# Optimization experiments

Hardware: AMD Instinct MI355X
Metric: run time of the kernel (lower is better)

Reference implementation:

```python
import jax, jax.numpy as jnp
import numpy as np

B, N, C_IN, C_Z, H = 1, 2048, 128, 16, 4
C = C_IN // H  # 32 per-head dim
QB, WL, WR = 32, 48, 80  # AF3 local atom attention: 32-query blocks, 128-key window


def _ln(x, eps=1e-5):
    m = jnp.mean(x, axis=-1, keepdims=True)
    v = jnp.mean((x - m) ** 2, axis=-1, keepdims=True)
    return (x - m) * jax.lax.rsqrt(v + eps)


def setup_inputs() -> dict:
    key = jax.random.key(0)
    ks = iter(jax.random.split(key, 32))
    def rn(shape, scale=0.02):
        return jax.random.normal(next(ks), shape, jnp.float32) * scale
    d = {}
    d['single_act'] = jax.random.normal(next(ks), (B, N, C_IN), jnp.float32)
    d['pair_act'] = jax.random.normal(next(ks), (B, N, N, C_Z), jnp.float32)
    d['single_cond'] = jax.random.normal(next(ks), (B, N, C_IN), jnp.float32)
    qi = jnp.arange(N)[:, None]
    kj = jnp.arange(N)[None, :]
    blk = (qi // QB) * QB
    d['block_mask'] = (kj >= blk - WL) & (kj < blk + WR)
    # AdaptiveLayerNorm params for q and k branches
    for p in ('q', 'k'):
        d[f'lns_{p}'] = jnp.ones((C_IN,), jnp.float32)       # LN(cond) scale (no bias)
        d[f'Wgate_{p}'] = rn((C_IN, C_IN))
        d[f'bgate_{p}'] = jnp.zeros((C_IN,), jnp.float32)
        d[f'Wskip_{p}'] = rn((C_IN, C_IN))
    d['lnz_w'] = jnp.ones((C_Z,), jnp.float32)               # layer_norm_z weight (bias=False)
    d['Wq'] = rn((C_IN, C_IN)); d['bq'] = jnp.zeros((C_IN,), jnp.float32)
    d['Wk'] = rn((C_IN, C_IN))
    d['Wv'] = rn((C_IN, C_IN))
    d['Wg'] = rn((C_IN, C_IN))
    d['Wb'] = rn((C_Z, H))
    # AdaptiveZeroInit: gated output projection, gate bias init -2
    d['Wo'] = rn((C_IN, C_IN))
    d['Wgs'] = rn((C_IN, C_IN))
    d['bgs'] = jnp.full((C_IN,), -2.0, jnp.float32)
    return d


def reference(single_act, pair_act, single_cond, block_mask,
              lns_q, Wgate_q, bgate_q, Wskip_q,
              lns_k, Wgate_k, bgate_k, Wskip_k,
              lnz_w, Wq, bq, Wk, Wv, Wg, Wb, Wo, Wgs, bgs):
    def adaln(x, s, lnsw, Wgt, bgt, Wsk):
        xn = _ln(x)                 # LN without affine
        sn = _ln(s) * lnsw          # LN with scale, no bias
        return jax.nn.sigmoid(sn @ Wgt + bgt) * xn + sn @ Wsk

    a_q = adaln(single_act, single_cond, lns_q, Wgate_q, bgate_q, Wskip_q)
    a_k = adaln(single_act, single_cond, lns_k, Wgate_k, bgate_k, Wskip_k)
    z = _ln(pair_act) * lnz_w                     # [B,N,N,Cz]

    q = (a_q @ Wq + bq).reshape(B, N, H, C)
    k = (a_k @ Wk).reshape(B, N, H, C)
    v = (a_k @ Wv).reshape(B, N, H, C)
    g = (a_q @ Wg).reshape(B, N, H, C)
    bias = z @ Wb                                 # [B,N,N,H]

    scores = jnp.einsum('bihc,bjhc->bhij', q, k) * (1.0 / np.sqrt(C).astype(np.float32))
    scores = scores + jnp.transpose(bias, (0, 3, 1, 2))
    scores = jnp.where(block_mask[None, None], scores, jnp.float32(-1e9))
    attn = jax.nn.softmax(scores, axis=-1)
    o = jnp.einsum('bhij,bjhc->bihc', attn, v)    # [B,N,H,C]
    o = (jax.nn.sigmoid(g) * o).reshape(B, N, C_IN)
    # AdaptiveZeroInit: sigmoid(Linear(cond)) * LinearNoBias(o)
    return jax.nn.sigmoid(single_cond @ Wgs + bgs) * (o @ Wo)
```

## Files before the change

### kernel.cpp

```cpp
#include <hip/hip_runtime.h>
#include <hip/hip_bf16.h>

#define NTOK 2048

typedef __attribute__((ext_vector_type(8))) short short8_t;
typedef __attribute__((ext_vector_type(4))) float f32x4;

__device__ __forceinline__ float bu2f(unsigned short u) {
  unsigned int x = ((unsigned int)u) << 16; float f; __builtin_memcpy(&f, &x, 4); return f;
}
__device__ __forceinline__ unsigned short f2bu(float f) {
  __hip_bfloat16 h = __float2bfloat16(f);
  unsigned short u; __builtin_memcpy(&u, &h, 2); return u;
}
__device__ __forceinline__ float sigm(float x) { return 1.0f / (1.0f + __expf(-x)); }
__device__ __forceinline__ uint4 pack8(const float* v) {
  unsigned short u[8];
#pragma unroll
  for (int i = 0; i < 8; ++i) u[i] = f2bu(v[i]);
  uint4 r; __builtin_memcpy(&r, u, 16); return r;
}
__device__ __forceinline__ short8_t pk8s(const float* v) {
  unsigned short u[8];
#pragma unroll
  for (int i = 0; i < 8; ++i) u[i] = f2bu(v[i]);
  short8_t r; __builtin_memcpy(&r, u, 16); return r;
}

__device__ __forceinline__ short8_t wfrag(const float* __restrict__ W,
                                          const float* __restrict__ lns,
                                          int ko, int n) {
  float v[8];
#pragma unroll
  for (int i = 0; i < 8; ++i) v[i] = W[(size_t)(ko + i) * 128 + n];
  if (lns) {
    float4 l0 = *(const float4*)(lns + ko);
    float4 l1 = *(const float4*)(lns + ko + 4);
    v[0] *= l0.x; v[1] *= l0.y; v[2] *= l0.z; v[3] *= l0.w;
    v[4] *= l1.x; v[5] *= l1.y; v[6] *= l1.z; v[7] *= l1.w;
  }
  return pk8s(v);
}

__device__ __forceinline__ void gemm_dw(const unsigned short* a_lds,
                                        const float* __restrict__ W,
                                        const float* __restrict__ lns,
                                        int lm, int kg, int wv, f32x4 acc[2][2]) {
  const int xa = (lm & 7) << 3;
#pragma unroll
  for (int ks = 0; ks < 4; ++ks) {
    const int ko = ks * 32 + kg * 8;
    short8_t av[2], bv[2];
#pragma unroll
    for (int mi = 0; mi < 2; ++mi)
      av[mi] = *(const short8_t*)&a_lds[(mi * 16 + lm) * 128 + (ko ^ xa)];
#pragma unroll
    for (int ni = 0; ni < 2; ++ni)
      bv[ni] = wfrag(W, lns, ko, (wv * 2 + ni) * 16 + lm);
#pragma unroll
    for (int mi = 0; mi < 2; ++mi)
#pragma unroll
      for (int ni = 0; ni < 2; ++ni)
        acc[mi][ni] = __builtin_amdgcn_mfma_f32_16x16x32_bf16(av[mi], bv[ni], acc[mi][ni], 0, 0, 0);
  }
}

__global__ __launch_bounds__(256) void bias_proj_kernel(
    const float* __restrict__ act, const float* __restrict__ cond,
    const float* __restrict__ lns_q, const float* __restrict__ lns_k,
    const float* __restrict__ WgQ, const float* __restrict__ WsQ,
    const float* __restrict__ WgK, const float* __restrict__ WsK,
    const float* __restrict__ Wq, const float* __restrict__ Wk,
    const float* __restrict__ Wv, const float* __restrict__ Wg,
    const float* __restrict__ Wgs,
    const float* __restrict__ bgate_q, const float* __restrict__ bgate_k,
    const float* __restrict__ bq, const float* __restrict__ bgs,
    const float* __restrict__ pair, const float* __restrict__ lnz_w,
    const float* __restrict__ Wb,
    unsigned short* __restrict__ q_b, unsigned short* __restrict__ k_b,
    unsigned short* __restrict__ vt_b, unsigned short* __restrict__ gsig_b,
    unsigned short* __restrict__ gs_b, unsigned short* __restrict__ bias_h)
{
  __shared__ unsigned short a_lds[32 * 128];
  __shared__ unsigned short xn_lds[32 * 136];
  __shared__ unsigned short a2_lds[32 * 128];
  __shared__ float lw[16];
  __shared__ float wbz[16][4];
  const int tid = threadIdx.x;
  const int bid = blockIdx.x;

  if (bid < 1024) {
    if (tid < 16) lw[tid] = lnz_w[tid];
    if (tid < 64) wbz[tid >> 2][tid & 3] = Wb[tid];
    __syncthreads();
    const int idx = bid * 256 + tid;
    const int i = idx >> 7, jw = idx & 127;
    const int j = ((i >> 5) << 5) - 48 + jw;
    float bo[4] = {-1e9f, -1e9f, -1e9f, -1e9f};
    if (j >= 0 && j < NTOK) {
      const float4* p = (const float4*)(pair + ((size_t)i * NTOK + j) * 16);
      float4 z0 = p[0], z1 = p[1], z2 = p[2], z3 = p[3];
      float z[16] = {z0.x, z0.y, z0.z, z0.w, z1.x, z1.y, z1.z, z1.w,
                     z2.x, z2.y, z2.z, z2.w, z3.x, z3.y, z3.z, z3.w};
      float s = 0.f, ss = 0.f;
#pragma unroll
      for (int c = 0; c < 16; ++c) { s += z[c]; ss += z[c]*z[c]; }
      const float m = s * (1.f/16.f), v = ss * (1.f/16.f) - m*m;
      const float r = rsqrtf(v + 1e-5f);
      bo[0] = bo[1] = bo[2] = bo[3] = 0.f;
#pragma unroll
      for (int c = 0; c < 16; ++c) {
        const float zn = (z[c] - m) * r * lw[c];
        bo[0] += zn * wbz[c][0]; bo[1] += zn * wbz[c][1];
        bo[2] += zn * wbz[c][2]; bo[3] += zn * wbz[c][3];
      }
    }
#pragma unroll
    for (int h = 0; h < 4; ++h)
      bias_h[(size_t)h * (NTOK * 128) + idx] = f2bu(bo[h]);
    return;
  }

  const int bb = bid - 1024;
  const int br = bb / 64;
  const int rt = bb % 64;
  const int row0 = rt * 32;
  const int l = tid & 63, wv = tid >> 6;
  const int lm = l & 15, kg = l >> 4;

  {
    const int r = tid >> 3;
    const int c0 = (tid & 7) << 4;
    float xv[16], cv[16];
    const float4* ap = (const float4*)(act + (size_t)(row0 + r) * 128 + c0);
    const float4* cp = (const float4*)(cond + (size_t)(row0 + r) * 128 + c0);
#pragma unroll
    for (int i = 0; i < 4; ++i) {
      float4 a4 = ap[i], b4 = cp[i];
      xv[4*i+0]=a4.x; xv[4*i+1]=a4.y; xv[4*i+2]=a4.z; xv[4*i+3]=a4.w;
      cv[4*i+0]=b4.x; cv[4*i+1]=b4.y; cv[4*i+2]=b4.z; cv[4*i+3]=b4.w;
    }
    float sx=0.f, sxx=0.f, sc=0.f, scc=0.f;
#pragma unroll
    for (int i = 0; i < 16; ++i) { sx+=xv[i]; sxx+=xv[i]*xv[i]; sc+=cv[i]; scc+=cv[i]*cv[i]; }
#pragma unroll
    for (int m = 1; m < 8; m <<= 1) {
      sx += __shfl_xor(sx, m); sxx += __shfl_xor(sxx, m);
      sc += __shfl_xor(sc, m); scc += __shfl_xor(scc, m);
    }
    const float mx = sx * (1.f/128.f), vx = sxx*(1.f/128.f) - mx*mx;
    const float mc = sc * (1.f/128.f), vc = scc*(1.f/128.f) - mc*mc;
    const float rx = rsqrtf(vx + 1e-5f), rc = rsqrtf(vc + 1e-5f);
    float xo[16], so[16];
#pragma unroll
    for (int i = 0; i < 16; ++i) { xo[i] = (xv[i]-mx)*rx; so[i] = (cv[i]-mc)*rc; }
    const int x = (r & 7) << 3;
    if (br == 4) {
      *(uint4*)&a_lds[r * 128 + (c0 ^ x)] = pack8(cv);
      *(uint4*)&a_lds[r * 128 + ((c0 + 8) ^ x)] = pack8(cv + 8);
    } else {
      *(uint4*)&a_lds[r * 128 + (c0 ^ x)] = pack8(so);
      *(uint4*)&a_lds[r * 128 + ((c0 + 8) ^ x)] = pack8(so + 8);
      *(uint4*)&xn_lds[r * 136 + c0] = pack8(xo);
      *(uint4*)&xn_lds[r * 136 + c0 + 8] = pack8(xo + 8);
    }
  }
  __syncthreads();

  if (br == 4) {
    f32x4 acc[2][2] = {};
    gemm_dw(a_lds, Wgs, nullptr, lm, kg, wv, acc);
    float bgv[2];
#pragma unroll
    for (int ni = 0; ni < 2; ++ni) bgv[ni] = bgs[(wv * 2 + ni) * 16 + lm];
#pragma unroll
    for (int mi = 0; mi < 2; ++mi)
#pragma unroll
      for (int ni = 0; ni < 2; ++ni)
#pragma unroll
        for (int r = 0; r < 4; ++r) {
          const int rl = mi * 16 + kg * 4 + r;
          const int n = (wv * 2 + ni) * 16 + lm;
          gs_b[(size_t)(row0 + rl) * 128 + n] = f2bu(sigm(acc[mi][ni][r] + bgv[ni]));
        }
    return;
  }

  const bool useq = (br < 2);
  const float* Wgt = useq ? WgQ : WgK;
  const float* Wsk = useq ? WsQ : WsK;
  const float* lns = useq ? lns_q : lns_k;
  const float* bg  = useq ? bgate_q : bgate_k;

  f32x4 ag[2][2] = {}, as2[2][2] = {};
  gemm_dw(a_lds, Wgt, lns, lm, kg, wv, ag);
  gemm_dw(a_lds, Wsk, lns, lm, kg, wv, as2);
  {
    float bgv[2];
#pragma unroll
    for (int ni = 0; ni < 2; ++ni) bgv[ni] = bg[(wv * 2 + ni) * 16 + lm];
#pragma unroll
    for (int mi = 0; mi < 2; ++mi)
#pragma unroll
      for (int ni = 0; ni < 2; ++ni)
#pragma unroll
        for (int r = 0; r < 4; ++r) {
          const int rl = mi * 16 + kg * 4 + r;
          const int n = (wv * 2 + ni) * 16 + lm;
          const float gate = sigm(ag[mi][ni][r] + bgv[ni]);
          const float a = gate * bu2f(xn_lds[rl * 136 + n]) + as2[mi][ni][r];
          a2_lds[rl * 128 + (n ^ ((rl & 7) << 3))] = f2bu(a);
        }
  }
  __syncthreads();

  const float* Wout = (br == 0) ? Wq : (br == 1) ? Wg : (br == 2) ? Wk : Wv;
  f32x4 ao[2][2] = {};
  gemm_dw(a2_lds, Wout, nullptr, lm, kg, wv, ao);

  if (br == 3) {
#pragma unroll
    for (int mi = 0; mi < 2; ++mi)
#pragma unroll
      for (int ni = 0; ni < 2; ++ni) {
        const int n = (wv * 2 + ni) * 16 + lm;
        const int tok0 = row0 + mi * 16 + kg * 4;
        ushort4 o;
        o.x = f2bu(ao[mi][ni][0]); o.y = f2bu(ao[mi][ni][1]);
        o.z = f2bu(ao[mi][ni][2]); o.w = f2bu(ao[mi][ni][3]);
        *(ushort4*)(vt_b + (size_t)n * NTOK + tok0) = o;
      }
    return;
  }
  const float scale = 0.17677669529663687f;
  float bqv[2] = {0.f, 0.f};
  if (br == 0) {
#pragma unroll
    for (int ni = 0; ni < 2; ++ni) bqv[ni] = bq[(wv * 2 + ni) * 16 + lm];
  }
  unsigned short* dst = (br == 0) ? q_b : (br == 1) ? gsig_b : k_b;
#pragma unroll
  for (int mi = 0; mi < 2; ++mi)
#pragma unroll
    for (int ni = 0; ni < 2; ++ni)
#pragma unroll
      for (int r = 0; r < 4; ++r) {
        const int rl = mi * 16 + kg * 4 + r;
        const int n = (wv * 2 + ni) * 16 + lm;
        float v = ao[mi][ni][r];
        if (br == 0) v = (v + bqv[ni]) * scale;
        else if (br == 1) v = sigm(v);
        dst[(size_t)(row0 + rl) * 128 + n] = f2bu(v);
      }
}

__global__ __launch_bounds__(256) void attn_kernel(
    const unsigned short* __restrict__ q_b, const unsigned short* __restrict__ k_b,
    const unsigned short* __restrict__ vt_b, const unsigned short* __restrict__ gsig_b,
    const unsigned short* __restrict__ bias_h, unsigned short* __restrict__ o_b)
{
  __shared__ unsigned short k_lds[128 * 64];
  __shared__ unsigned short vt[32 * 128];
  __shared__ unsigned short p_lds[32 * 128];
  __shared__ unsigned short q_lds[32 * 64];
  __shared__ unsigned short bias_lds[32 * 136];
  __shared__ float mxlds[4][32];
  __shared__ float smlds[4][32];
  __shared__ f32x4 op[16][64];
  const int tid = threadIdx.x;
  const int h = blockIdx.x & 3, b = blockIdx.x >> 2;
  const int j0 = b * 32 - 48;
  const int l = tid & 63, wv = tid >> 6;
  const int lm = l & 15, kg = l >> 4;

  {
    const int r = tid >> 3, c0 = (tid & 7) << 2;
    ushort4 v = *(const ushort4*)(q_b + (size_t)(b * 32 + r) * 128 + h * 32 + c0);
    *(ushort4*)&q_lds[r * 64 + (c0 ^ ((r & 7) << 3))] = v;
  }
  {
    const int r = tid >> 3, c0 = (tid & 7) << 4;
    const uint4* g = (const uint4*)(bias_h + (size_t)h * (NTOK * 128) + (size_t)(b * 32 + r) * 128 + c0);
    uint4 v0 = g[0], v1 = g[1];
    *(uint4*)&bias_lds[r * 136 + c0] = v0;
    *(uint4*)&bias_lds[r * 136 + c0 + 8] = v1;
  }
  {
    const int jw = tid >> 1, cb = (tid & 1) << 4;
    const int j = j0 + jw;
    uint4 kv0 = {0,0,0,0}, kv1 = {0,0,0,0};
    if (j >= 0 && j < NTOK) {
      const uint4* gk = (const uint4*)(k_b + (size_t)j * 128 + h * 32 + cb);
      kv0 = gk[0]; kv1 = gk[1];
    }
    const int xk = (jw & 7) << 3;
    *(uint4*)&k_lds[jw * 64 + (cb ^ xk)] = kv0;
    *(uint4*)&k_lds[jw * 64 + ((cb + 8) ^ xk)] = kv1;
  }
  {
    const int c = tid >> 3, koff = (tid & 7) << 4;
    const int j = j0 + koff;
    uint4 v0 = {0,0,0,0}, v1 = {0,0,0,0};
    if (j >= 0 && j + 15 < NTOK) {
      const uint4* gv = (const uint4*)(vt_b + (size_t)(h * 32 + c) * NTOK + j);
      v0 = gv[0]; v1 = gv[1];
    }
    const int xc = (c & 7) << 3;
    *(uint4*)&vt[c * 128 + (koff ^ xc)] = v0;
    *(uint4*)&vt[c * 128 + ((koff + 8) ^ xc)] = v1;
  }
  __syncthreads();

  f32x4 sc[2][2] = {};
  {
    const int xa = (lm & 7) << 3;
    short8_t aq[2], bk[2];
#pragma unroll
    for (int mi = 0; mi < 2; ++mi)
      aq[mi] = *(const short8_t*)&q_lds[(mi * 16 + lm) * 64 + ((kg * 8) ^ xa)];
#pragma unroll
    for (int ni = 0; ni < 2; ++ni) {
      const int key = (wv * 2 + ni) * 16 + lm;
      bk[ni] = *(const short8_t*)&k_lds[key * 64 + ((kg * 8) ^ ((key & 7) << 3))];
    }
#pragma unroll
    for (int mi = 0; mi < 2; ++mi)
#pragma unroll
      for (int ni = 0; ni < 2; ++ni)
        sc[mi][ni] = __builtin_amdgcn_mfma_f32_16x16x32_bf16(aq[mi], bk[ni], sc[mi][ni], 0, 0, 0);
  }
  float sv[2][2][4];
#pragma unroll
  for (int mi = 0; mi < 2; ++mi)
#pragma unroll
    for (int ni = 0; ni < 2; ++ni)
#pragma unroll
      for (int r = 0; r < 4; ++r) {
        const int q = mi * 16 + kg * 4 + r;
        const int key = (wv * 2 + ni) * 16 + lm;
        sv[mi][ni][r] = sc[mi][ni][r] + bu2f(bias_lds[q * 136 + key]);
      }
#pragma unroll
  for (int mi = 0; mi < 2; ++mi)
#pragma unroll
    for (int r = 0; r < 4; ++r) {
      float m0 = fmaxf(sv[mi][0][r], sv[mi][1][r]);
#pragma unroll
      for (int msk = 1; msk < 16; msk <<= 1) m0 = fmaxf(m0, __shfl_xor(m0, msk));
      if (lm == 0) mxlds[wv][mi * 16 + kg * 4 + r] = m0;
    }
  __syncthreads();
#pragma unroll
  for (int mi = 0; mi < 2; ++mi)
#pragma unroll
    for (int r = 0; r < 4; ++r) {
      const int q = mi * 16 + kg * 4 + r;
      const float m = fmaxf(fmaxf(mxlds[0][q], mxlds[1][q]), fmaxf(mxlds[2][q], mxlds[3][q]));
      float s = 0.f;
#pragma unroll
      for (int ni = 0; ni < 2; ++ni) {
        const float e = __expf(sv[mi][ni][r] - m);
        const int key = (wv * 2 + ni) * 16 + lm;
        p_lds[q * 128 + ((key & 7) | ((key & 120) ^ ((q & 7) << 3)))] = f2bu(e);
        s += e;
      }
#pragma unroll
      for (int msk = 1; msk < 16; msk <<= 1) s += __shfl_xor(s, msk);
      if (lm == 0) smlds[wv][q] = s;
    }
  f32x4 oacc[2][2] = {};
  {
    const int key0 = wv * 32 + kg * 8;
    short8_t pa[2], vbf[2];
#pragma unroll
    for (int mi = 0; mi < 2; ++mi) {
      const int q = mi * 16 + lm;
      pa[mi] = *(const short8_t*)&p_lds[q * 128 + (key0 ^ ((q & 7) << 3))];
    }
#pragma unroll
    for (int ct = 0; ct < 2; ++ct) {
      const int c = ct * 16 + lm;
      vbf[ct] = *(const short8_t*)&vt[c * 128 + (key0 ^ ((c & 7) << 3))];
    }
#pragma unroll
    for (int mi = 0; mi < 2; ++mi)
#pragma unroll
      for (int ct = 0; ct < 2; ++ct)
        oacc[mi][ct] = __builtin_amdgcn_mfma_f32_16x16x32_bf16(pa[mi], vbf[ct], oacc[mi][ct], 0, 0, 0);
  }
#pragma unroll
  for (int mi = 0; mi < 2; ++mi)
#pragma unroll
    for (int ct = 0; ct < 2; ++ct)
      op[wv * 4 + mi * 2 + ct][l] = oacc[mi][ct];
  __syncthreads();
  {
    const int q = tid >> 3, c0 = (tid & 7) << 2;
    const int mt = q >> 4, g = (q >> 2) & 3, r = q & 3;
    const float tot = smlds[0][q] + smlds[1][q] + smlds[2][q] + smlds[3][q];
    const float inv = 1.f / tot;
    ushort4 gg = *(const ushort4*)(gsig_b + (size_t)(b * 32 + q) * 128 + h * 32 + c0);
    unsigned short gga[4] = {gg.x, gg.y, gg.z, gg.w};
    unsigned short outa[4];
#pragma unroll
    for (int i2 = 0; i2 < 4; ++i2) {
      const int c = c0 + i2;
      const int ct = c >> 4, lane = g * 16 + (c & 15);
      float s = 0.f;
#pragma unroll
      for (int w2 = 0; w2 < 4; ++w2)
        s += ((const float*)&op[w2 * 4 + mt * 2 + ct][lane])[r];
      outa[i2] = f2bu(s * inv * bu2f(gga[i2]));
    }
    ushort4 ov; ov.x = outa[0]; ov.y = outa[1]; ov.z = outa[2]; ov.w = outa[3];
    *(ushort4*)(o_b + (size_t)(b * 32 + q) * 128 + h * 32 + c0) = ov;
  }
}

__global__ __launch_bounds__(256) void out_kernel(
    const float* __restrict__ Wo, const unsigned short* __restrict__ o_b,
    const unsigned short* __restrict__ gs_b, float* __restrict__ out)
{
  __shared__ unsigned short a_lds[16 * 128];
  const int tid = threadIdx.x;
  const int row0 = blockIdx.x * 16;
  const int l = tid & 63, wv = tid >> 6;
  const int lm = l & 15, kg = l >> 4;
  {
    const int r = tid >> 4, c0 = (tid & 15) << 3;
    uint4 v = *(const uint4*)(o_b + (size_t)(row0 + r) * 128 + c0);
    *(uint4*)&a_lds[r * 128 + (c0 ^ ((r & 7) << 3))] = v;
  }
  __syncthreads();
  f32x4 acc[2] = {};
  const int xa = (lm & 7) << 3;
#pragma unroll
  for (int ks = 0; ks < 4; ++ks) {
    const int ko = ks * 32 + kg * 8;
    short8_t av = *(const short8_t*)&a_lds[lm * 128 + (ko ^ xa)];
#pragma unroll
    for (int ni = 0; ni < 2; ++ni) {
      short8_t bv = wfrag(Wo, nullptr, ko, (wv * 2 + ni) * 16 + lm);
      acc[ni] = __builtin_amdgcn_mfma_f32_16x16x32_bf16(av, bv, acc[ni], 0, 0, 0);
    }
  }
#pragma unroll
  for (int ni = 0; ni < 2; ++ni)
#pragma unroll
    for (int r = 0; r < 4; ++r) {
      const int rl = kg * 4 + r;
      const int n = (wv * 2 + ni) * 16 + lm;
      const float gsv = bu2f(gs_b[(size_t)(row0 + rl) * 128 + n]);
      out[(size_t)(row0 + rl) * 128 + n] = acc[ni][r] * gsv;
    }
}

extern "C" void kernel_launch(void* const* d_in, const int* in_sizes, int n_in,
                              void* d_out, int out_size, void* d_ws, size_t ws_size,
                              hipStream_t stream) {
  const float* act     = (const float*)d_in[0];
  const float* pair    = (const float*)d_in[1];
  const float* cond    = (const float*)d_in[2];
  const float* lns_q   = (const float*)d_in[4];
  const float* Wgate_q = (const float*)d_in[5];
  const float* bgate_q = (const float*)d_in[6];
  const float* Wskip_q = (const float*)d_in[7];
  const float* lns_k   = (const float*)d_in[8];
  const float* Wgate_k = (const float*)d_in[9];
  const float* bgate_k = (const float*)d_in[10];
  const float* Wskip_k = (const float*)d_in[11];
  const float* lnz_w   = (const float*)d_in[12];
  const float* Wq      = (const float*)d_in[13];
  const float* bq      = (const float*)d_in[14];
  const float* Wk      = (const float*)d_in[15];
  const float* Wv      = (const float*)d_in[16];
  const float* Wg      = (const float*)d_in[17];
  const float* Wb      = (const float*)d_in[18];
  const float* Wo      = (const float*)d_in[19];
  const float* Wgs     = (const float*)d_in[20];
  const float* bgs     = (const float*)d_in[21];
  float* out           = (float*)d_out;

  unsigned short* ws = (unsigned short*)d_ws;
  unsigned short* q_b    = ws;
  unsigned short* k_b    = ws + 262144;
  unsigned short* vt_b   = ws + 524288;
  unsigned short* gsig_b = ws + 786432;
  unsigned short* gs_b   = ws + 1048576;
  unsigned short* o_b    = ws + 1310720;
  unsigned short* bias_h = ws + 1572864;

  hipLaunchKernelGGL(bias_proj_kernel, dim3(1344), dim3(256), 0, stream,
                     act, cond, lns_q, lns_k,
                     Wgate_q, Wskip_q, Wgate_k, Wskip_k,
                     Wq, Wk, Wv, Wg, Wgs,
                     bgate_q, bgate_k, bq, bgs,
                     pair, lnz_w, Wb,
                     q_b, k_b, vt_b, gsig_b, gs_b, bias_h);
  hipLaunchKernelGGL(attn_kernel, dim3(256), dim3(256), 0, stream,
                     q_b, k_b, vt_b, gsig_b, bias_h, o_b);
  hipLaunchKernelGGL(out_kernel, dim3(128), dim3(256), 0, stream,
                     Wo, o_b, gs_b, out);
}
```

Measured before the change: 27.02 us.

## Fuse output projection into attention kernel via per-head atomic accumulation

Removes the separate out_kernel. Each attention block now multiplies its per-head 32x32 output tile by the matching Wo slice and atomically adds the gated partial products into the final output. The output is zeroed inside the first kernel. This saves one kernel launch and the o_b round trip through global memory, at the cost of four float atomics per output element from the four head blocks and nondeterministic summation order.

```diff
diff --git a/kernel.cpp b/kernel.cpp
--- a/kernel.cpp
+++ b/kernel.cpp
@@ -79,7 +79,8 @@
     const float* __restrict__ Wb,
     unsigned short* __restrict__ q_b, unsigned short* __restrict__ k_b,
     unsigned short* __restrict__ vt_b, unsigned short* __restrict__ gsig_b,
-    unsigned short* __restrict__ gs_b, unsigned short* __restrict__ bias_h)
+    unsigned short* __restrict__ gs_b, unsigned short* __restrict__ bias_h,
+    float* __restrict__ out)
 {
   __shared__ unsigned short a_lds[32 * 128];
   __shared__ unsigned short xn_lds[32 * 136];
@@ -90,6 +91,7 @@
   const int bid = blockIdx.x;
 
   if (bid < 1024) {
+    out[(size_t)bid * 256 + tid] = 0.f;
     if (tid < 16) lw[tid] = lnz_w[tid];
     if (tid < 64) wbz[tid >> 2][tid & 3] = Wb[tid];
     __syncthreads();
@@ -257,7 +259,8 @@
 __global__ __launch_bounds__(256) void attn_kernel(
     const unsigned short* __restrict__ q_b, const unsigned short* __restrict__ k_b,
     const unsigned short* __restrict__ vt_b, const unsigned short* __restrict__ gsig_b,
-    const unsigned short* __restrict__ bias_h, unsigned short* __restrict__ o_b)
+    const unsigned short* __restrict__ bias_h, const unsigned short* __restrict__ gs_b,
+    const float* __restrict__ Wo, float* __restrict__ out)
 {
   __shared__ unsigned short k_lds[128 * 64];
   __shared__ unsigned short vt[32 * 128];
@@ -267,6 +270,7 @@
   __shared__ float mxlds[4][32];
   __shared__ float smlds[4][32];
   __shared__ f32x4 op[16][64];
+  __shared__ unsigned short o_lds[32 * 40];
   const int tid = threadIdx.x;
   const int h = blockIdx.x & 3, b = blockIdx.x >> 2;
   const int j0 = b * 32 - 48;
@@ -413,46 +417,36 @@
       outa[i2] = f2bu(s * inv * bu2f(gga[i2]));
     }
     ushort4 ov; ov.x = outa[0]; ov.y = outa[1]; ov.z = outa[2]; ov.w = outa[3];
-    *(ushort4*)(o_b + (size_t)(b * 32 + q) * 128 + h * 32 + c0) = ov;
-  }
-}
-
-__global__ __launch_bounds__(256) void out_kernel(
-    const float* __restrict__ Wo, const unsigned short* __restrict__ o_b,
-    const unsigned short* __restrict__ gs_b, float* __restrict__ out)
-{
-  __shared__ unsigned short a_lds[16 * 128];
-  const int tid = threadIdx.x;
-  const int row0 = blockIdx.x * 16;
-  const int l = tid & 63, wv = tid >> 6;
-  const int lm = l & 15, kg = l >> 4;
-  {
-    const int r = tid >> 4, c0 = (tid & 15) << 3;
-    uint4 v = *(const uint4*)(o_b + (size_t)(row0 + r) * 128 + c0);
-    *(uint4*)&a_lds[r * 128 + (c0 ^ ((r & 7) << 3))] = v;
-  }
-  __syncthreads();
-  f32x4 acc[2] = {};
-  const int xa = (lm & 7) << 3;
-#pragma unroll
-  for (int ks = 0; ks < 4; ++ks) {
-    const int ko = ks * 32 + kg * 8;
-    short8_t av = *(const short8_t*)&a_lds[lm * 128 + (ko ^ xa)];
-#pragma unroll
-    for (int ni = 0; ni < 2; ++ni) {
-      short8_t bv = wfrag(Wo, nullptr, ko, (wv * 2 + ni) * 16 + lm);
-      acc[ni] = __builtin_amdgcn_mfma_f32_16x16x32_bf16(av, bv, acc[ni], 0, 0, 0);
-    }
-  }
-#pragma unroll
-  for (int ni = 0; ni < 2; ++ni)
-#pragma unroll
-    for (int r = 0; r < 4; ++r) {
-      const int rl = kg * 4 + r;
-      const int n = (wv * 2 + ni) * 16 + lm;
-      const float gsv = bu2f(gs_b[(size_t)(row0 + rl) * 128 + n]);
-      out[(size_t)(row0 + rl) * 128 + n] = acc[ni][r] * gsv;
-    }
+    *(ushort4*)&o_lds[q * 40 + c0] = ov;
+  }
+  __syncthreads();
+
+  {
+    short8_t av[2], bv[2];
+#pragma unroll
+    for (int mi = 0; mi < 2; ++mi)
+      av[mi] = *(const short8_t*)&o_lds[(mi * 16 + lm) * 40 + kg * 8];
+#pragma unroll
+    for (int ni = 0; ni < 2; ++ni)
+      bv[ni] = wfrag(Wo, nullptr, h * 32 + kg * 8, (wv * 2 + ni) * 16 + lm);
+    f32x4 pacc[2][2] = {};
+#pragma unroll
+    for (int mi = 0; mi < 2; ++mi)
+#pragma unroll
+      for (int ni = 0; ni < 2; ++ni)
+        pacc[mi][ni] = __builtin_amdgcn_mfma_f32_16x16x32_bf16(av[mi], bv[ni], pacc[mi][ni], 0, 0, 0);
+#pragma unroll
+    for (int mi = 0; mi < 2; ++mi)
+#pragma unroll
+      for (int ni = 0; ni < 2; ++ni)
+#pragma unroll
+        for (int r = 0; r < 4; ++r) {
+          const int row = b * 32 + mi * 16 + kg * 4 + r;
+          const int n = (wv * 2 + ni) * 16 + lm;
+          const float gsv = bu2f(gs_b[(size_t)row * 128 + n]);
+          atomicAdd(&out[(size_t)row * 128 + n], gsv * pacc[mi][ni][r]);
+        }
+  }
 }
 
 extern "C" void kernel_launch(void* const* d_in, const int* in_sizes, int n_in,
@@ -487,8 +481,7 @@
   unsigned short* vt_b   = ws + 524288;
   unsigned short* gsig_b = ws + 786432;
   unsigned short* gs_b   = ws + 1048576;
-  unsigned short* o_b    = ws + 1310720;
-  unsigned short* bias_h = ws + 1572864;
+  unsigned short* bias_h = ws + 1310720;
 
   hipLaunchKernelGGL(bias_proj_kernel, dim3(1344), dim3(256), 0, stream,
                      act, cond, lns_q, lns_k,
@@ -496,9 +489,7 @@
                      Wq, Wk, Wv, Wg, Wgs,
                      bgate_q, bgate_k, bq, bgs,
                      pair, lnz_w, Wb,
-                     q_b, k_b, vt_b, gsig_b, gs_b, bias_h);
+                     q_b, k_b, vt_b, gsig_b, gs_b, bias_h, out);
   hipLaunchKernelGGL(attn_kernel, dim3(256), dim3(256), 0, stream,
-                     q_b, k_b, vt_b, gsig_b, bias_h, o_b);
-  hipLaunchKernelGGL(out_kernel, dim3(128), dim3(256), 0, stream,
-                     Wo, o_b, gs_b, out);
-}
+                     q_b, k_b, vt_b, gsig_b, bias_h, gs_b, Wo, out);
+}
```

After: 31.02 us. 1.15x slower.
